# Optimization experiments

Measured on AMD Instinct MI355X. Metric: run time of the kernel, lower is better.

Reference implementation:

```python
import jax, jax.numpy as jnp
import numpy as np

B, S, D, H = 4, 2048, 1024, 16
DH = D // H  # per-head depth = 64


def setup_inputs() -> dict:
    key = jax.random.key(0)
    kq, kk, kv = jax.random.split(key, 3)
    q = jax.random.normal(kq, (B, S, D), dtype=jnp.float32)
    k = jax.random.normal(kk, (B, S, D), dtype=jnp.float32)
    v = jax.random.normal(kv, (B, S, D), dtype=jnp.float32)
    # Standard look-ahead mask: 1.0 where attention is disallowed (j > i).
    mask = (1.0 - jnp.tril(jnp.ones((S, S), dtype=jnp.float32)))[None, None, :, :]
    return {"q": q, "k": k, "v": v, "mask": mask, "training": 0}


def _split_heads(x):
    # [B, S, D] -> [B, H, S, DH]
    b, s, _ = x.shape
    return x.reshape(b, s, H, DH).transpose(0, 2, 1, 3)


def reference(q, k, v, mask, training):
    qh, kh, vh = _split_heads(q), _split_heads(k), _split_heads(v)
    scale = 1.0 / jnp.sqrt(jnp.float32(DH))
    logits = jnp.einsum("bhqd,bhkd->bhqk", qh, kh) * scale  # [B,H,S,S]
    logits = logits + mask * (-1e9)
    weights = jax.nn.softmax(logits, axis=-1)
    attn = jnp.einsum("bhqk,bhkd->bhqd", weights, vh)  # [B,H,S,DH]
    out = attn.transpose(0, 2, 1, 3).reshape(q.shape[0], 1, -1, H * DH)  # [B,1,S,D]
    return out
```

## Files before the change

kernel.cpp:

```cpp
#include <hip/hip_runtime.h>
#include <hip/hip_bf16.h>


constexpr int Ss = 2048, Dd = 1024, Hh = 16, DH = 64, Bb = 4;
constexpr float QSCALE = 0.125f * 1.44269504088896f;
constexpr float MFIX2 = 13.0f;
constexpr float MFIXF = 9.0f;

typedef _Float16 half2_t __attribute__((ext_vector_type(2)));
typedef _Float16 half4_t __attribute__((ext_vector_type(4)));
typedef _Float16 half8_t __attribute__((ext_vector_type(8)));
typedef __attribute__((ext_vector_type(4))) float floatx4;
typedef __attribute__((ext_vector_type(8))) short short8;

union H8 { half8_t v; half2_t h2[4]; };

__device__ __forceinline__ half2_t pk(float a, float b) {
  return __builtin_bit_cast(half2_t, __builtin_amdgcn_cvt_pkrtz(a, b));
}
__device__ __forceinline__ float fexp2(float x) {
#if __has_builtin(__builtin_amdgcn_exp2f)
  return __builtin_amdgcn_exp2f(x);
#else
  return __exp2f(x);
#endif
}
__device__ __forceinline__ unsigned short f2bf(float f) {
  union { float f; unsigned u; } x; x.f = f;
  unsigned r = x.u + 0x7FFFu + ((x.u >> 16) & 1u);
  return (unsigned short)(r >> 16);
}
__device__ __forceinline__ unsigned short f2bf_trunc(float f) {
  union { float f; unsigned u; } x; x.f = f;
  return (unsigned short)(x.u >> 16);
}
__device__ __forceinline__ void async_cp16(const unsigned short* g, unsigned short* l) {
  __builtin_amdgcn_global_load_lds(
      (const __attribute__((address_space(1))) unsigned int*)g,
      (__attribute__((address_space(3))) unsigned int*)l, 16, 0, 0);
}

__global__ __launch_bounds__(256)
void prep_kv(const float* __restrict__ Kg, const float* __restrict__ Vg,
             unsigned short* __restrict__ Kh, unsigned short* __restrict__ Vt) {
  __shared__ float tile[64][65];
  const int s0 = (int)blockIdx.x * 64;
  const int bh = (int)blockIdx.y;
  const int b = bh >> 4, h = bh & 15;
  const int t = threadIdx.x;
  const int sl = t >> 2, qtr = t & 3;

  const size_t inoff = ((size_t)(b * Ss + s0 + sl)) * Dd + h * DH + qtr * 16;
  const float* krow = Kg + inoff;
  const float* vrow = Vg + inoff;
  const int pout = (2 * (sl >> 5) + ((sl & 7) >> 2)) * 16 + ((sl >> 3) & 3) * 4 + (sl & 3);
  unsigned short* kout = Kh + ((size_t)bh * Ss + s0 + pout) * 64 + qtr * 16;

  #pragma unroll
  for (int i = 0; i < 2; ++i) {
    float4 k0 = ((const float4*)krow)[i * 2 + 0];
    float4 k1 = ((const float4*)krow)[i * 2 + 1];
    H8 o;
    o.h2[0] = pk(k0.x, k0.y); o.h2[1] = pk(k0.z, k0.w);
    o.h2[2] = pk(k1.x, k1.y); o.h2[3] = pk(k1.z, k1.w);
    *(half8_t*)(kout + i * 8) = o.v;
  }
  #pragma unroll
  for (int i = 0; i < 4; ++i) {
    float4 v = ((const float4*)vrow)[i];
    tile[sl][qtr * 16 + i * 4 + 0] = v.x;
    tile[sl][qtr * 16 + i * 4 + 1] = v.y;
    tile[sl][qtr * 16 + i * 4 + 2] = v.z;
    tile[sl][qtr * 16 + i * 4 + 3] = v.w;
  }
  __syncthreads();
  const int d = t >> 2, kc = t & 3;
  unsigned short* orow = Vt + ((size_t)bh * DH + d) * Ss + s0 + kc * 16;
  #pragma unroll
  for (int i = 0; i < 2; ++i) {
    H8 o;
    o.h2[0] = pk(tile[kc * 16 + i * 8 + 0][d], tile[kc * 16 + i * 8 + 1][d]);
    o.h2[1] = pk(tile[kc * 16 + i * 8 + 2][d], tile[kc * 16 + i * 8 + 3][d]);
    o.h2[2] = pk(tile[kc * 16 + i * 8 + 4][d], tile[kc * 16 + i * 8 + 5][d]);
    o.h2[3] = pk(tile[kc * 16 + i * 8 + 6][d], tile[kc * 16 + i * 8 + 7][d]);
    *(half8_t*)(orow + i * 8) = o.v;
  }
}

__global__ __launch_bounds__(256, 2)
void mha_fa8(const float* __restrict__ Qg, const unsigned short* __restrict__ Kh,
             const unsigned short* __restrict__ Vt, float* __restrict__ Og) {
  __shared__ __align__(16) unsigned short Kld[2][128 * 64];
  __shared__ __align__(16) unsigned short Vld[2][64 * 128];

  const int tid = threadIdx.x;
  const int wave = tid >> 6, lane = tid & 63;
  const int c = lane & 15, qd = lane >> 4;
  const int bh = (int)blockIdx.x;
  const int b = bh >> 4, h = bh & 15;
  const int slot = (int)blockIdx.y;
  const int t = (slot < 4) ? slot : 11 - slot;
  const int Qt[2] = {2 * t + 1, 2 * t};
  const int nkt = 2 * t + 2;

  const unsigned short* kbase = Kh + (size_t)bh * Ss * 64;
  const unsigned short* vbase = Vt + (size_t)bh * DH * Ss;
  float* obase = Og + (size_t)b * Ss * Dd + h * DH;

  auto stage = [&](int kt, int bufi) {
    const unsigned short* ktile = kbase + kt * 128 * 64;
    #pragma unroll
    for (int it = 0; it < 4; ++it) {
      int p = (it * 4 + wave) * 64 + lane;
      int r = p >> 3, pos = p & 7, j = pos ^ (r & 7);
      async_cp16(ktile + r * 64 + j * 8, &Kld[bufi][(it * 4 + wave) * 512]);
    }
    #pragma unroll
    for (int it = 0; it < 4; ++it) {
      int p = (it * 4 + wave) * 64 + lane;
      int d = p >> 4, c16 = p & 15;
      int j = (c16 & 8) | ((c16 ^ d) & 7);
      async_cp16(vbase + (size_t)d * Ss + kt * 128 + j * 8,
                 &Vld[bufi][(it * 4 + wave) * 512]);
    }
  };

  const half8_t ones8 = {(_Float16)1.f, (_Float16)1.f, (_Float16)1.f, (_Float16)1.f,
                         (_Float16)1.f, (_Float16)1.f, (_Float16)1.f, (_Float16)1.f};

  half8_t qf[2][2][2];
  #pragma unroll
  for (int ti = 0; ti < 2; ++ti) {
    #pragma unroll
    for (int mi = 0; mi < 2; ++mi) {
      const float* qr =
          Qg + ((size_t)b * Ss + Qt[ti] * 128 + mi * 64 + wave * 16 + c) * Dd + h * DH;
      #pragma unroll
      for (int ks = 0; ks < 2; ++ks) {
        float4 a0 = ((const float4*)(qr + ks * 32 + qd * 8))[0];
        float4 a1 = ((const float4*)(qr + ks * 32 + qd * 8))[1];
        H8 f;
        f.h2[0] = pk(a0.x * QSCALE, a0.y * QSCALE);
        f.h2[1] = pk(a0.z * QSCALE, a0.w * QSCALE);
        f.h2[2] = pk(a1.x * QSCALE, a1.y * QSCALE);
        f.h2[3] = pk(a1.z * QSCALE, a1.w * QSCALE);
        qf[ti][mi][ks] = f.v;
      }
    }
  }

  floatx4 o_acc[2][2][4];
  floatx4 l_acc[2][2];
  #pragma unroll
  for (int ti = 0; ti < 2; ++ti)
    #pragma unroll
    for (int mi = 0; mi < 2; ++mi) {
      #pragma unroll
      for (int f = 0; f < 4; ++f) o_acc[ti][mi][f] = (floatx4){0.f, 0.f, 0.f, 0.f};
      l_acc[ti][mi] = (floatx4){0.f, 0.f, 0.f, 0.f};
    }

  stage(0, 0);

  for (int kt = 0; kt < nkt; ++kt) {
    __syncthreads();
    const int bufi = kt & 1;
    if (kt + 1 < nkt) stage(kt + 1, bufi ^ 1);

    const unsigned short* Kl = Kld[bufi];
    const unsigned short* Vl = Vld[bufi];

    #pragma unroll
    for (int kb = 0; kb < 2; ++kb) {
      const int kb0 = kt * 128 + kb * 64;

      half8_t kf0[4], kf1[4];
      #pragma unroll
      for (int f = 0; f < 4; ++f) {
        int kk = kb * 64 + f * 16 + c;
        kf0[f] = *(const half8_t*)&Kl[kk * 64 + (qd ^ (c & 7)) * 8];
        kf1[f] = *(const half8_t*)&Kl[kk * 64 + ((4 + qd) ^ (c & 7)) * 8];
      }
      half8_t w8[4][2];
      #pragma unroll
      for (int f = 0; f < 4; ++f) {
        int rr = f * 16 + c;
        #pragma unroll
        for (int wnd = 0; wnd < 2; ++wnd) {
          int chi = kb * 8 + wnd * 4 + qd;
          int phys = (chi & 8) | ((chi ^ rr) & 7);
          w8[f][wnd] = *(const half8_t*)&Vl[rr * 128 + phys * 8];
        }
      }

      #pragma unroll
      for (int ti = 0; ti < 2; ++ti) {
        #pragma unroll
        for (int mi = 0; mi < 2; ++mi) {
          const int qlo = Qt[ti] * 128 + mi * 64 + wave * 16;
          if (kb0 > qlo + 15) continue;

          floatx4 s[4];
          #pragma unroll
          for (int f = 0; f < 4; ++f) s[f] = (floatx4){0.f, 0.f, 0.f, 0.f};
          #pragma unroll
          for (int f = 0; f < 4; ++f) {
            s[f] = __builtin_amdgcn_mfma_f32_16x16x32_f16(kf0[f], qf[ti][mi][0], s[f], 0, 0, 0);
            s[f] = __builtin_amdgcn_mfma_f32_16x16x32_f16(kf1[f], qf[ti][mi][1], s[f], 0, 0, 0);
          }
          if (kb0 + 63 > qlo) {
            #pragma unroll
            for (int f = 0; f < 4; ++f) {
              int keyb = kb0 + ((f >> 1) << 5) + ((f & 1) << 2) + qd * 8;
              #pragma unroll
              for (int r = 0; r < 4; ++r)
                if (keyb + r > qlo + c) s[f][r] = -1e30f;
            }
          }
          half8_t p8[2];
          #pragma unroll
          for (int wnd = 0; wnd < 2; ++wnd) {
            H8 pp;
            pp.h2[0] = pk(fexp2(s[2 * wnd][0] - MFIX2), fexp2(s[2 * wnd][1] - MFIX2));
            pp.h2[1] = pk(fexp2(s[2 * wnd][2] - MFIX2), fexp2(s[2 * wnd][3] - MFIX2));
            pp.h2[2] = pk(fexp2(s[2 * wnd + 1][0] - MFIX2), fexp2(s[2 * wnd + 1][1] - MFIX2));
            pp.h2[3] = pk(fexp2(s[2 * wnd + 1][2] - MFIX2), fexp2(s[2 * wnd + 1][3] - MFIX2));
            p8[wnd] = pp.v;
          }
          #pragma unroll
          for (int fd = 0; fd < 4; ++fd) {
            #pragma unroll
            for (int wnd = 0; wnd < 2; ++wnd)
              o_acc[ti][mi][fd] = __builtin_amdgcn_mfma_f32_16x16x32_f16(
                  p8[wnd], w8[fd][wnd], o_acc[ti][mi][fd], 0, 0, 0);
          }
          #pragma unroll
          for (int wnd = 0; wnd < 2; ++wnd)
            l_acc[ti][mi] = __builtin_amdgcn_mfma_f32_16x16x32_f16(p8[wnd], ones8,
                                                                   l_acc[ti][mi], 0, 0, 0);
        }
      }
    }
  }

  #pragma unroll
  for (int ti = 0; ti < 2; ++ti)
    #pragma unroll
    for (int mi = 0; mi < 2; ++mi)
      #pragma unroll
      for (int r = 0; r < 4; ++r) {
        float inv = 1.f / l_acc[ti][mi][r];
        size_t row = (size_t)(Qt[ti] * 128 + mi * 64 + wave * 16 + qd * 4 + r);
        #pragma unroll
        for (int f = 0; f < 4; ++f)
          obase[row * Dd + f * 16 + c] = o_acc[ti][mi][f][r] * inv;
      }
}

__global__ __launch_bounds__(256, 4)
void mha_fwd(const float* __restrict__ Qg, const float* __restrict__ Kg,
             const float* __restrict__ Vg, float* __restrict__ Og) {
  __shared__ __align__(16) unsigned short Kldf[64 * 72];
  __shared__ __align__(16) unsigned short Vtldf[64 * 72];
  __shared__ __align__(16) unsigned short Pldf[4 * 16 * 72];
  const int tid = threadIdx.x, wave = tid >> 6, lane = tid & 63;
  const int c = lane & 15, qd = lane >> 4;
  const int qt = (Ss / 64 - 1) - (int)blockIdx.x;
  const int b = (int)blockIdx.y >> 4, h = (int)blockIdx.y & 15;
  const float* qbase = Qg + (size_t)b * Ss * Dd + h * DH;
  const float* kbase = Kg + (size_t)b * Ss * Dd + h * DH;
  const float* vbase = Vg + (size_t)b * Ss * Dd + h * DH;
  short8 qfrag[2];
  {
    const float* qr = qbase + (size_t)(qt * 64 + wave * 16 + c) * Dd + qd * 8;
    for (int ks = 0; ks < 2; ++ks) {
      float4 a0 = ((const float4*)(qr + ks * 32))[0];
      float4 a1 = ((const float4*)(qr + ks * 32))[1];
      short8 f;
      f[0] = (short)f2bf(a0.x * 0.125f); f[1] = (short)f2bf(a0.y * 0.125f);
      f[2] = (short)f2bf(a0.z * 0.125f); f[3] = (short)f2bf(a0.w * 0.125f);
      f[4] = (short)f2bf(a1.x * 0.125f); f[5] = (short)f2bf(a1.y * 0.125f);
      f[6] = (short)f2bf(a1.z * 0.125f); f[7] = (short)f2bf(a1.w * 0.125f);
      qfrag[ks] = f;
    }
  }
  floatx4 o_acc[4];
  for (int f = 0; f < 4; ++f) o_acc[f] = (floatx4){0.f, 0.f, 0.f, 0.f};
  float l_lane[4] = {0.f, 0.f, 0.f, 0.f};
  const int row_g = qt * 64 + wave * 16;
  const int pbase = wave * 16 * 72;
  for (int kt = 0; kt <= qt; ++kt) {
    __syncthreads();
    {
      const int r = tid >> 2, quarter = tid & 3;
      const float* krow = kbase + (size_t)(kt * 64 + r) * Dd + quarter * 16;
      const float* vrow = vbase + (size_t)(kt * 64 + r) * Dd + quarter * 16;
      for (int i = 0; i < 4; ++i) {
        float4 kv = ((const float4*)krow)[i];
        int col = quarter * 16 + i * 4;
        ushort4 kk;
        kk.x = f2bf(kv.x); kk.y = f2bf(kv.y); kk.z = f2bf(kv.z); kk.w = f2bf(kv.w);
        *(ushort4*)&Kldf[r * 72 + col] = kk;
        float4 vv = ((const float4*)vrow)[i];
        Vtldf[(col + 0) * 72 + r] = f2bf(vv.x);
        Vtldf[(col + 1) * 72 + r] = f2bf(vv.y);
        Vtldf[(col + 2) * 72 + r] = f2bf(vv.z);
        Vtldf[(col + 3) * 72 + r] = f2bf(vv.w);
      }
    }
    __syncthreads();
    floatx4 s_acc[4];
    for (int f = 0; f < 4; ++f) s_acc[f] = (floatx4){0.f, 0.f, 0.f, 0.f};
    for (int f = 0; f < 4; ++f)
      for (int ks = 0; ks < 2; ++ks) {
        short8 kf = *(const short8*)&Kldf[(f * 16 + c) * 72 + ks * 32 + qd * 8];
        s_acc[f] = __builtin_amdgcn_mfma_f32_16x16x32_bf16(qfrag[ks], kf, s_acc[f], 0, 0, 0);
      }
    if (kt == qt)
      for (int f = 0; f < 4; ++f) {
        int key = kt * 64 + f * 16 + c;
        for (int r = 0; r < 4; ++r)
          if (key > row_g + qd * 4 + r) s_acc[f][r] = -1e30f;
      }
    for (int f = 0; f < 4; ++f)
      for (int r = 0; r < 4; ++r) {
        float p = __expf(s_acc[f][r] - MFIXF);
        l_lane[r] += p;
        Pldf[pbase + (qd * 4 + r) * 72 + f * 16 + c] = f2bf_trunc(p);
      }
    short8 pfrag[2];
    pfrag[0] = *(const short8*)&Pldf[pbase + c * 72 + qd * 8];
    pfrag[1] = *(const short8*)&Pldf[pbase + c * 72 + 32 + qd * 8];
    for (int f = 0; f < 4; ++f)
      for (int ks = 0; ks < 2; ++ks) {
        short8 vf = *(const short8*)&Vtldf[(f * 16 + c) * 72 + ks * 32 + qd * 8];
        o_acc[f] = __builtin_amdgcn_mfma_f32_16x16x32_bf16(pfrag[ks], vf, o_acc[f], 0, 0, 0);
      }
  }
  float* obase = Og + (size_t)b * Ss * Dd + h * DH;
  for (int r = 0; r < 4; ++r) {
    float lv = l_lane[r];
    lv += __shfl_xor(lv, 1); lv += __shfl_xor(lv, 2);
    lv += __shfl_xor(lv, 4); lv += __shfl_xor(lv, 8);
    float inv_l = 1.f / lv;
    size_t rowoff = (size_t)(row_g + qd * 4 + r) * Dd;
    for (int f = 0; f < 4; ++f)
      obase[rowoff + f * 16 + c] = o_acc[f][r] * inv_l;
  }
}

extern "C" void kernel_launch(void* const* d_in, const int* in_sizes, int n_in,
                              void* d_out, int out_size, void* d_ws, size_t ws_size,
                              hipStream_t stream) {
  const float* q = (const float*)d_in[0];
  const float* k = (const float*)d_in[1];
  const float* v = (const float*)d_in[2];
  float* out = (float*)d_out;

  const size_t elems = (size_t)Bb * Hh * Ss * DH;
  if (ws_size >= 2 * elems * 2) {
    unsigned short* kh = (unsigned short*)d_ws;
    unsigned short* vt = kh + elems;
    prep_kv<<<dim3(Ss / 64, Bb * Hh), 256, 0, stream>>>(k, v, kh, vt);
    mha_fa8<<<dim3(Bb * Hh, 8), 256, 0, stream>>>(q, kh, vt, out);
  } else {
    mha_fwd<<<dim3(Ss / 64, Bb * Hh), 256, 0, stream>>>(q, k, v, out);
  }
}
```

Measured before the change: 200.3 us.

## Restructure K/V double-buffer pipeline with early prefetch and MFMA priority hints

Prefetches two K/V tiles up front and replaces the per-iteration __syncthreads with explicit vmcnt waits plus raw barriers. The next-next tile is issued mid-iteration, once the second half's fragments are in registers, so the global-to-LDS copy overlaps the second half's compute. It also raises wave priority around the MFMA blocks with s_setprio so the matrix units stay busy. This relies on hand-counted vmcnt values (8 outstanding copies per stage) and raises register pressure, which could cause races or spills if the counts are wrong.

```diff
diff --git a/kernel.cpp b/kernel.cpp
--- a/kernel.cpp
+++ b/kernel.cpp
@@ -88,7 +88,7 @@
 }
 
 __global__ __launch_bounds__(256, 2)
-void mha_fa8(const float* __restrict__ Qg, const unsigned short* __restrict__ Kh,
+void mha_fa9(const float* __restrict__ Qg, const unsigned short* __restrict__ Kh,
              const unsigned short* __restrict__ Vt, float* __restrict__ Og) {
   __shared__ __align__(16) unsigned short Kld[2][128 * 64];
   __shared__ __align__(16) unsigned short Vld[2][64 * 128];
@@ -125,6 +125,26 @@
     }
   };
 
+  auto load_frags = [&](const unsigned short* Kl, const unsigned short* Vl, int kb,
+                        half8_t (&kf0)[4], half8_t (&kf1)[4], half8_t (&w8)[4][2]) {
+    #pragma unroll
+    for (int f = 0; f < 4; ++f) {
+      int kk = kb * 64 + f * 16 + c;
+      kf0[f] = *(const half8_t*)&Kl[kk * 64 + (qd ^ (c & 7)) * 8];
+      kf1[f] = *(const half8_t*)&Kl[kk * 64 + ((4 + qd) ^ (c & 7)) * 8];
+    }
+    #pragma unroll
+    for (int f = 0; f < 4; ++f) {
+      int rr = f * 16 + c;
+      #pragma unroll
+      for (int wnd = 0; wnd < 2; ++wnd) {
+        int chi = kb * 8 + wnd * 4 + qd;
+        int phys = (chi & 8) | ((chi ^ rr) & 7);
+        w8[f][wnd] = *(const half8_t*)&Vl[rr * 128 + phys * 8];
+      }
+    }
+  };
+
   const half8_t ones8 = {(_Float16)1.f, (_Float16)1.f, (_Float16)1.f, (_Float16)1.f,
                          (_Float16)1.f, (_Float16)1.f, (_Float16)1.f, (_Float16)1.f};
 
@@ -160,87 +180,88 @@
       l_acc[ti][mi] = (floatx4){0.f, 0.f, 0.f, 0.f};
     }
 
+  auto compute_kb = [&](int kb0g, const half8_t (&kf0)[4], const half8_t (&kf1)[4],
+                        const half8_t (&w8)[4][2]) {
+    #pragma unroll
+    for (int ti = 0; ti < 2; ++ti) {
+      #pragma unroll
+      for (int mi = 0; mi < 2; ++mi) {
+        const int qlo = Qt[ti] * 128 + mi * 64 + wave * 16;
+        if (kb0g > qlo + 15) continue;
+
+        floatx4 s[4];
+        #pragma unroll
+        for (int f = 0; f < 4; ++f) s[f] = (floatx4){0.f, 0.f, 0.f, 0.f};
+        __builtin_amdgcn_s_setprio(1);
+        #pragma unroll
+        for (int f = 0; f < 4; ++f) {
+          s[f] = __builtin_amdgcn_mfma_f32_16x16x32_f16(kf0[f], qf[ti][mi][0], s[f], 0, 0, 0);
+          s[f] = __builtin_amdgcn_mfma_f32_16x16x32_f16(kf1[f], qf[ti][mi][1], s[f], 0, 0, 0);
+        }
+        __builtin_amdgcn_s_setprio(0);
+        if (kb0g + 63 > qlo) {
+          #pragma unroll
+          for (int f = 0; f < 4; ++f) {
+            int keyb = kb0g + ((f >> 1) << 5) + ((f & 1) << 2) + qd * 8;
+            #pragma unroll
+            for (int r = 0; r < 4; ++r)
+              if (keyb + r > qlo + c) s[f][r] = -1e30f;
+          }
+        }
+        half8_t p8[2];
+        #pragma unroll
+        for (int wnd = 0; wnd < 2; ++wnd) {
+          H8 pp;
+          pp.h2[0] = pk(fexp2(s[2 * wnd][0] - MFIX2), fexp2(s[2 * wnd][1] - MFIX2));
+          pp.h2[1] = pk(fexp2(s[2 * wnd][2] - MFIX2), fexp2(s[2 * wnd][3] - MFIX2));
+          pp.h2[2] = pk(fexp2(s[2 * wnd + 1][0] - MFIX2), fexp2(s[2 * wnd + 1][1] - MFIX2));
+          pp.h2[3] = pk(fexp2(s[2 * wnd + 1][2] - MFIX2), fexp2(s[2 * wnd + 1][3] - MFIX2));
+          p8[wnd] = pp.v;
+        }
+        __builtin_amdgcn_s_setprio(1);
+        #pragma unroll
+        for (int fd = 0; fd < 4; ++fd) {
+          #pragma unroll
+          for (int wnd = 0; wnd < 2; ++wnd)
+            o_acc[ti][mi][fd] = __builtin_amdgcn_mfma_f32_16x16x32_f16(
+                p8[wnd], w8[fd][wnd], o_acc[ti][mi][fd], 0, 0, 0);
+        }
+        #pragma unroll
+        for (int wnd = 0; wnd < 2; ++wnd)
+          l_acc[ti][mi] = __builtin_amdgcn_mfma_f32_16x16x32_f16(p8[wnd], ones8,
+                                                                 l_acc[ti][mi], 0, 0, 0);
+        __builtin_amdgcn_s_setprio(0);
+      }
+    }
+  };
+
+  asm volatile("s_waitcnt vmcnt(0)" ::: "memory");
   stage(0, 0);
+  stage(1, 1);
 
   for (int kt = 0; kt < nkt; ++kt) {
-    __syncthreads();
     const int bufi = kt & 1;
-    if (kt + 1 < nkt) stage(kt + 1, bufi ^ 1);
+    if (kt + 1 < nkt) {
+      asm volatile("s_waitcnt vmcnt(8)" ::: "memory");
+    } else {
+      asm volatile("s_waitcnt vmcnt(0)" ::: "memory");
+    }
+    __builtin_amdgcn_s_barrier();
 
     const unsigned short* Kl = Kld[bufi];
     const unsigned short* Vl = Vld[bufi];
 
-    #pragma unroll
-    for (int kb = 0; kb < 2; ++kb) {
-      const int kb0 = kt * 128 + kb * 64;
-
-      half8_t kf0[4], kf1[4];
-      #pragma unroll
-      for (int f = 0; f < 4; ++f) {
-        int kk = kb * 64 + f * 16 + c;
-        kf0[f] = *(const half8_t*)&Kl[kk * 64 + (qd ^ (c & 7)) * 8];
-        kf1[f] = *(const half8_t*)&Kl[kk * 64 + ((4 + qd) ^ (c & 7)) * 8];
-      }
-      half8_t w8[4][2];
-      #pragma unroll
-      for (int f = 0; f < 4; ++f) {
-        int rr = f * 16 + c;
-        #pragma unroll
-        for (int wnd = 0; wnd < 2; ++wnd) {
-          int chi = kb * 8 + wnd * 4 + qd;
-          int phys = (chi & 8) | ((chi ^ rr) & 7);
-          w8[f][wnd] = *(const half8_t*)&Vl[rr * 128 + phys * 8];
-        }
-      }
-
-      #pragma unroll
-      for (int ti = 0; ti < 2; ++ti) {
-        #pragma unroll
-        for (int mi = 0; mi < 2; ++mi) {
-          const int qlo = Qt[ti] * 128 + mi * 64 + wave * 16;
-          if (kb0 > qlo + 15) continue;
-
-          floatx4 s[4];
-          #pragma unroll
-          for (int f = 0; f < 4; ++f) s[f] = (floatx4){0.f, 0.f, 0.f, 0.f};
-          #pragma unroll
-          for (int f = 0; f < 4; ++f) {
-            s[f] = __builtin_amdgcn_mfma_f32_16x16x32_f16(kf0[f], qf[ti][mi][0], s[f], 0, 0, 0);
-            s[f] = __builtin_amdgcn_mfma_f32_16x16x32_f16(kf1[f], qf[ti][mi][1], s[f], 0, 0, 0);
-          }
-          if (kb0 + 63 > qlo) {
-            #pragma unroll
-            for (int f = 0; f < 4; ++f) {
-              int keyb = kb0 + ((f >> 1) << 5) + ((f & 1) << 2) + qd * 8;
-              #pragma unroll
-              for (int r = 0; r < 4; ++r)
-                if (keyb + r > qlo + c) s[f][r] = -1e30f;
-            }
-          }
-          half8_t p8[2];
-          #pragma unroll
-          for (int wnd = 0; wnd < 2; ++wnd) {
-            H8 pp;
-            pp.h2[0] = pk(fexp2(s[2 * wnd][0] - MFIX2), fexp2(s[2 * wnd][1] - MFIX2));
-            pp.h2[1] = pk(fexp2(s[2 * wnd][2] - MFIX2), fexp2(s[2 * wnd][3] - MFIX2));
-            pp.h2[2] = pk(fexp2(s[2 * wnd + 1][0] - MFIX2), fexp2(s[2 * wnd + 1][1] - MFIX2));
-            pp.h2[3] = pk(fexp2(s[2 * wnd + 1][2] - MFIX2), fexp2(s[2 * wnd + 1][3] - MFIX2));
-            p8[wnd] = pp.v;
-          }
-          #pragma unroll
-          for (int fd = 0; fd < 4; ++fd) {
-            #pragma unroll
-            for (int wnd = 0; wnd < 2; ++wnd)
-              o_acc[ti][mi][fd] = __builtin_amdgcn_mfma_f32_16x16x32_f16(
-                  p8[wnd], w8[fd][wnd], o_acc[ti][mi][fd], 0, 0, 0);
-          }
-          #pragma unroll
-          for (int wnd = 0; wnd < 2; ++wnd)
-            l_acc[ti][mi] = __builtin_amdgcn_mfma_f32_16x16x32_f16(p8[wnd], ones8,
-                                                                   l_acc[ti][mi], 0, 0, 0);
-        }
-      }
-    }
+    half8_t kf0a[4], kf1a[4], w8a[4][2];
+    load_frags(Kl, Vl, 0, kf0a, kf1a, w8a);
+    compute_kb(kt * 128, kf0a, kf1a, w8a);
+
+    half8_t kf0b[4], kf1b[4], w8b[4][2];
+    load_frags(Kl, Vl, 1, kf0b, kf1b, w8b);
+    asm volatile("s_waitcnt lgkmcnt(0)" ::: "memory");
+    __builtin_amdgcn_s_barrier();
+    if (kt + 2 < nkt) stage(kt + 2, bufi);
+
+    compute_kb(kt * 128 + 64, kf0b, kf1b, w8b);
   }
 
   #pragma unroll
@@ -362,7 +383,7 @@
     unsigned short* kh = (unsigned short*)d_ws;
     unsigned short* vt = kh + elems;
     prep_kv<<<dim3(Ss / 64, Bb * Hh), 256, 0, stream>>>(k, v, kh, vt);
-    mha_fa8<<<dim3(Bb * Hh, 8), 256, 0, stream>>>(q, kh, vt, out);
+    mha_fa9<<<dim3(Bb * Hh, 8), 256, 0, stream>>>(q, kh, vt, out);
   } else {
     mha_fwd<<<dim3(Ss / 64, Bb * Hh), 256, 0, stream>>>(q, k, v, out);
   }
```

After: 201.9 us. No clear change (+0.8%).
